# Kernel tuning notes

Hardware: AMD Instinct MI355X
Metric: run time of the kernel (lower is better)

The kernel has to match this reference:

```python
import jax, jax.numpy as jnp
import numpy as np

N_NODES = 100000
N_FEAT = 256
N_EDGES = 3200000
N_CLUSTERS = 16
COLLAPSE_REG = 0.1


def setup_inputs() -> dict:
    key = jax.random.key(0)
    k1, k2, k3, k4 = jax.random.split(key, 4)
    features = jax.random.normal(k1, (N_NODES, N_FEAT), dtype=jnp.float32)
    edge_row = jax.random.randint(k2, (N_EDGES,), 0, N_NODES, dtype=jnp.int32)
    edge_col = jax.random.randint(k3, (N_EDGES,), 0, N_NODES, dtype=jnp.int32)
    edge_val = jnp.ones((N_EDGES,), dtype=jnp.float32)
    # orthogonal-ish init approximated by scaled normal (init does not affect math)
    W = jax.random.normal(k4, (N_FEAT, N_CLUSTERS), dtype=jnp.float32) / np.float32(np.sqrt(N_FEAT))
    b = jnp.zeros((N_CLUSTERS,), dtype=jnp.float32)
    return {"features": features, "W": W, "b": b,
            "edge_row": edge_row, "edge_col": edge_col, "edge_val": edge_val}


def reference(features, W, b, edge_row, edge_col, edge_val):
    n = features.shape[0]
    k = W.shape[1]
    # assignment softmax (dropout_rate=0 -> identity)
    assignments = jax.nn.softmax(features @ W + b, axis=1)  # [n, k]
    cluster_sizes = assignments.sum(axis=0)                  # [k]
    assignments_pooling = assignments / cluster_sizes        # [n, k]
    # degrees = sparse row sums of adjacency
    degrees = jax.ops.segment_sum(edge_val, edge_row, num_segments=n)[:, None]  # [n, 1]
    n_edges = degrees.sum() / 2
    # sparse mm: adjacency @ assignments via gather + segment_sum
    adj_assign = jax.ops.segment_sum(edge_val[:, None] * assignments[edge_col],
                                     edge_row, num_segments=n)  # [n, k]
    graph_pooled = assignments.T @ adj_assign                # [k, k]
    normalizer_left = assignments.T @ degrees                # [k, 1]
    normalizer_right = degrees.T @ assignments               # [1, k]
    normalizer = normalizer_left @ normalizer_right / (2 * n_edges)
    spectral_loss = -jnp.trace(graph_pooled - normalizer) / (2 * n_edges)
    collapse_loss = COLLAPSE_REG * (jnp.linalg.norm(cluster_sizes) / n
                                    * jnp.sqrt(jnp.float32(k)) - 1.0)
    features_pooled = jax.nn.selu(assignments_pooling.T @ features)  # [k, d]
    return features_pooled, assignments, spectral_loss, collapse_loss
```

## Files before the change

kernel.cpp:

```cpp
#include <hip/hip_runtime.h>
#include <math.h>

#define KC 16
#define DF 256

#define WS_POOLED 0
#define WS_CS     4096
#define WS_M      4112
#define WS_TR     4128
#define WS_ESUM   4129
#define WS_TOTAL  4130
#define SHDW_OFF_BYTES 16640


typedef float floatx2 __attribute__((ext_vector_type(2)));

__global__ void zero_ws_kernel(float* __restrict__ ws) {
  int i = blockIdx.x * blockDim.x + threadIdx.x;
  if (i < WS_TOTAL) ws[i] = 0.0f;
}

__device__ __forceinline__ void cvt16_fp8(uint4 u, float* f) {
  floatx2 p;
  p = __builtin_amdgcn_cvt_pk_f32_fp8(u.x, false); f[0] = p[0];  f[1] = p[1];
  p = __builtin_amdgcn_cvt_pk_f32_fp8(u.x, true);  f[2] = p[0];  f[3] = p[1];
  p = __builtin_amdgcn_cvt_pk_f32_fp8(u.y, false); f[4] = p[0];  f[5] = p[1];
  p = __builtin_amdgcn_cvt_pk_f32_fp8(u.y, true);  f[6] = p[0];  f[7] = p[1];
  p = __builtin_amdgcn_cvt_pk_f32_fp8(u.z, false); f[8] = p[0];  f[9] = p[1];
  p = __builtin_amdgcn_cvt_pk_f32_fp8(u.z, true);  f[10] = p[0]; f[11] = p[1];
  p = __builtin_amdgcn_cvt_pk_f32_fp8(u.w, false); f[12] = p[0]; f[13] = p[1];
  p = __builtin_amdgcn_cvt_pk_f32_fp8(u.w, true);  f[14] = p[0]; f[15] = p[1];
}

__device__ __forceinline__ void acc_edge1(uint4 A, uint4 B, float vq,
                                          float* m, float& tr, float& es) {
  float a[16], bb[16];
  cvt16_fp8(A, a); cvt16_fp8(B, bb);
  float d = 0.f;
  #pragma unroll
  for (int k = 0; k < 16; ++k) d += a[k] * bb[k];
  tr += vq * d; es += vq;
  #pragma unroll
  for (int k = 0; k < 16; ++k) m[k] += vq * a[k];
}

__global__ void __launch_bounds__(256, 2) assign_kernel(
    const float* __restrict__ F, const float* __restrict__ W,
    const float* __restrict__ b, float* __restrict__ S,
    unsigned* __restrict__ Sh, float* __restrict__ ws, int n) {
  __shared__ float Ft[2][32 * 257];
  __shared__ float cs_l[KC];
  const int t = threadIdx.x;
  if (t < KC) cs_l[t] = 0.0f;
  const int nb = blockIdx.x << 8;
  const int node = nb + t;
  const bool valid = node < n;
  const bool interior = (nb + 256 <= n);

  const int nl = t >> 3;
  const int jc = t & 7;

  float4 pref[8];
  auto load_chunk = [&](int s) {
    #pragma unroll
    for (int it = 0; it < 8; ++it) {
      const int nn = nl + (it << 5);
      if (interior || nb + nn < n)
        pref[it] = *(const float4*)&F[(size_t)(nb + nn) * DF + (s << 5) + (jc << 2)];
      else
        pref[it] = make_float4(0.f, 0.f, 0.f, 0.f);
    }
  };

  float acc[KC];
  #pragma unroll
  for (int k = 0; k < KC; ++k) acc[k] = 0.f;

  load_chunk(0);
  for (int s = 0; s < 8; ++s) {
    float* __restrict__ B = Ft[s & 1];
    #pragma unroll
    for (int it = 0; it < 8; ++it) {
      const int nn = nl + (it << 5);
      const int d0 = jc << 2;
      B[(d0 + 0) * 257 + nn] = pref[it].x;
      B[(d0 + 1) * 257 + nn] = pref[it].y;
      B[(d0 + 2) * 257 + nn] = pref[it].z;
      B[(d0 + 3) * 257 + nn] = pref[it].w;
    }
    __syncthreads();
    if (s < 7) load_chunk(s + 1);
    #pragma unroll
    for (int j = 0; j < 8; ++j) {
      const float fv0 = B[(4 * j + 0) * 257 + t];
      const float fv1 = B[(4 * j + 1) * 257 + t];
      const float fv2 = B[(4 * j + 2) * 257 + t];
      const float fv3 = B[(4 * j + 3) * 257 + t];
      const float* __restrict__ Wg = &W[(size_t)((s << 5) + (j << 2)) * KC];
      #pragma unroll
      for (int k = 0; k < KC; ++k)
        acc[k] += fv0 * Wg[k] + fv1 * Wg[KC + k]
                + fv2 * Wg[2 * KC + k] + fv3 * Wg[3 * KC + k];
    }
  }

  float mx = -1e30f;
  #pragma unroll
  for (int k = 0; k < KC; ++k) { acc[k] += b[k]; mx = fmaxf(mx, acc[k]); }
  float sum = 0.f;
  #pragma unroll
  for (int k = 0; k < KC; ++k) { acc[k] = __expf(acc[k] - mx); sum += acc[k]; }
  const float inv = 1.0f / sum;
  #pragma unroll
  for (int k = 0; k < KC; ++k) acc[k] *= inv;
  if (!valid) {
    #pragma unroll
    for (int k = 0; k < KC; ++k) acc[k] = 0.f;
  }
  if (valid) {
    float4* __restrict__ So = (float4*)&S[(size_t)node * KC];
    So[0] = make_float4(acc[0],  acc[1],  acc[2],  acc[3]);
    So[1] = make_float4(acc[4],  acc[5],  acc[6],  acc[7]);
    So[2] = make_float4(acc[8],  acc[9],  acc[10], acc[11]);
    So[3] = make_float4(acc[12], acc[13], acc[14], acc[15]);
    if (Sh) {
      unsigned w0, w1, w2, w3;
      w0 = __builtin_amdgcn_cvt_pk_fp8_f32(acc[0],  acc[1],  0,  false);
      w0 = __builtin_amdgcn_cvt_pk_fp8_f32(acc[2],  acc[3],  w0, true);
      w1 = __builtin_amdgcn_cvt_pk_fp8_f32(acc[4],  acc[5],  0,  false);
      w1 = __builtin_amdgcn_cvt_pk_fp8_f32(acc[6],  acc[7],  w1, true);
      w2 = __builtin_amdgcn_cvt_pk_fp8_f32(acc[8],  acc[9],  0,  false);
      w2 = __builtin_amdgcn_cvt_pk_fp8_f32(acc[10], acc[11], w2, true);
      w3 = __builtin_amdgcn_cvt_pk_fp8_f32(acc[12], acc[13], 0,  false);
      w3 = __builtin_amdgcn_cvt_pk_fp8_f32(acc[14], acc[15], w3, true);
      *(uint4*)&Sh[(size_t)node * 4] = make_uint4(w0, w1, w2, w3);
    }
  }
  #pragma unroll
  for (int off = 1; off < 64; off <<= 1) {
    #pragma unroll
    for (int k = 0; k < KC; ++k) acc[k] += __shfl_xor(acc[k], off);
  }
  if ((t & 63) == 0) {
    #pragma unroll
    for (int k = 0; k < KC; ++k) atomicAdd(&cs_l[k], acc[k]);
  }
  __syncthreads();
  if (t < KC) atomicAdd(&ws[WS_CS + t], cs_l[t]);
}

__device__ __forceinline__ void edge_body_fp8(
    const int* __restrict__ erow, const int* __restrict__ ecol,
    const float* __restrict__ evl, const uint4* __restrict__ S8,
    float* __restrict__ ws, int ne, int idx, float* __restrict__ red) {
  const int t = threadIdx.x;
  if (t < KC + 2) red[t] = 0.0f;
  __syncthreads();

  float m[KC];
  #pragma unroll
  for (int i = 0; i < KC; ++i) m[i] = 0.f;
  float tr = 0.f, es = 0.f;

  const int cbase = idx << 11;
  const int base = cbase + t;
  int r[8], c[8];
  float v[8];
  if (cbase + 2048 <= ne) {
    #pragma unroll
    for (int i = 0; i < 8; ++i) {
      const int e = base + (i << 8);
      r[i] = erow[e]; c[i] = ecol[e]; v[i] = evl[e];
    }
  } else {
    #pragma unroll
    for (int i = 0; i < 8; ++i) {
      const int e = base + (i << 8);
      const bool ok = e < ne;
      r[i] = ok ? erow[e] : 0;
      c[i] = ok ? ecol[e] : 0;
      v[i] = ok ? evl[e] : 0.f;
    }
  }

  const uint4 A0 = S8[r[0]], B0 = S8[c[0]], A1 = S8[r[1]], B1 = S8[c[1]],
              A2 = S8[r[2]], B2 = S8[c[2]], A3 = S8[r[3]], B3 = S8[c[3]],
              A4 = S8[r[4]], B4 = S8[c[4]], A5 = S8[r[5]], B5 = S8[c[5]],
              A6 = S8[r[6]], B6 = S8[c[6]], A7 = S8[r[7]], B7 = S8[c[7]];
  acc_edge1(A0, B0, v[0], m, tr, es);
  acc_edge1(A1, B1, v[1], m, tr, es);
  acc_edge1(A2, B2, v[2], m, tr, es);
  acc_edge1(A3, B3, v[3], m, tr, es);
  acc_edge1(A4, B4, v[4], m, tr, es);
  acc_edge1(A5, B5, v[5], m, tr, es);
  acc_edge1(A6, B6, v[6], m, tr, es);
  acc_edge1(A7, B7, v[7], m, tr, es);

  #pragma unroll
  for (int off = 1; off < 64; off <<= 1) {
    tr += __shfl_xor(tr, off);
    es += __shfl_xor(es, off);
    #pragma unroll
    for (int i = 0; i < KC; ++i) m[i] += __shfl_xor(m[i], off);
  }
  if ((t & 63) == 0) {
    atomicAdd(&red[KC], tr);
    atomicAdd(&red[KC + 1], es);
    #pragma unroll
    for (int i = 0; i < KC; ++i) atomicAdd(&red[i], m[i]);
  }
  __syncthreads();
  if (t < KC)            atomicAdd(&ws[WS_M + t], red[t]);
  else if (t == KC)      atomicAdd(&ws[WS_TR], red[KC]);
  else if (t == KC + 1)  atomicAdd(&ws[WS_ESUM], red[KC + 1]);
}

__device__ __forceinline__ void pool_body(
    const float* __restrict__ F, const float* __restrict__ S,
    float* __restrict__ ws, int n, int idx, int pg) {
  const int t = threadIdx.x;
  float acc[KC];
  #pragma unroll
  for (int i = 0; i < KC; ++i) acc[i] = 0.f;

  const int nch = n >> 5;
  for (int ch = idx; ch < nch; ch += pg) {
    const int base = ch << 5;
    float fl[32];
    #pragma unroll
    for (int i = 0; i < 32; ++i)
      fl[i] = F[(size_t)(base + i) * DF + t];
    #pragma unroll
    for (int i = 0; i < 32; ++i) {
      const float4* __restrict__ Sr = (const float4*)(S + (size_t)(base + i) * KC);
      const float4 s0 = Sr[0], s1 = Sr[1], s2 = Sr[2], s3 = Sr[3];
      const float f = fl[i];
      acc[0]+=f*s0.x;  acc[1]+=f*s0.y;  acc[2]+=f*s0.z;  acc[3]+=f*s0.w;
      acc[4]+=f*s1.x;  acc[5]+=f*s1.y;  acc[6]+=f*s1.z;  acc[7]+=f*s1.w;
      acc[8]+=f*s2.x;  acc[9]+=f*s2.y;  acc[10]+=f*s2.z; acc[11]+=f*s2.w;
      acc[12]+=f*s3.x; acc[13]+=f*s3.y; acc[14]+=f*s3.z; acc[15]+=f*s3.w;
    }
  }
  if (idx == 0) {
    for (int i2 = nch << 5; i2 < n; ++i2) {
      const float f = F[(size_t)i2 * DF + t];
      const float* __restrict__ Sr = S + (size_t)i2 * KC;
      #pragma unroll
      for (int kk = 0; kk < KC; ++kk) acc[kk] += f * Sr[kk];
    }
  }
  const int rot = idx & 15;
  #pragma unroll
  for (int kk = 0; kk < KC; ++kk) {
    const int kidx = (kk + rot) & 15;
    atomicAdd(&ws[WS_POOLED + kidx * DF + t], acc[kidx]);
  }
}

__global__ void __launch_bounds__(256) edge_pool_kernel(
    const int* __restrict__ erow, const int* __restrict__ ecol,
    const float* __restrict__ evl, const uint4* __restrict__ S8,
    const float* __restrict__ F, const float* __restrict__ S,
    float* __restrict__ ws, int ne, int n, int pg, int eg) {
  __shared__ float red[KC + 2];
  const int bid = blockIdx.x;
  const int mn = pg < eg ? pg : eg;
  const int nInter = 2 * mn;
  int role, idx;
  if (bid < nInter) { role = bid & 1; idx = bid >> 1; }
  else {
    const int rem = bid - nInter;
    role = (pg > eg) ? 0 : 1;
    idx = mn + rem;
  }
  if (role == 0) pool_body(F, S, ws, n, idx, pg);
  else           edge_body_fp8(erow, ecol, evl, S8, ws, ne, idx, red);
}

__global__ void __launch_bounds__(256) edge_kernel_f32(
    const int* __restrict__ erow, const int* __restrict__ ecol,
    const float* __restrict__ evl, const float* __restrict__ S,
    float* __restrict__ ws, int ne) {
  __shared__ float red[KC + 2];
  const int t = threadIdx.x;
  if (t < KC + 2) red[t] = 0.0f;
  __syncthreads();
  float m[KC];
  #pragma unroll
  for (int i = 0; i < KC; ++i) m[i] = 0.f;
  float tr = 0.f, es = 0.f;
  const int stride = gridDim.x * blockDim.x;
  for (int e = blockIdx.x * blockDim.x + t; e < ne; e += stride) {
    const int r = erow[e];
    const int c = ecol[e];
    const float v = evl[e];
    const float4* __restrict__ Sr = (const float4*)(S + (size_t)r * KC);
    const float4* __restrict__ Sc = (const float4*)(S + (size_t)c * KC);
    const float4 a0 = Sr[0], a1 = Sr[1], a2 = Sr[2], a3 = Sr[3];
    const float4 b0 = Sc[0], b1 = Sc[1], b2 = Sc[2], b3 = Sc[3];
    float d = a0.x*b0.x + a0.y*b0.y + a0.z*b0.z + a0.w*b0.w
            + a1.x*b1.x + a1.y*b1.y + a1.z*b1.z + a1.w*b1.w
            + a2.x*b2.x + a2.y*b2.y + a2.z*b2.z + a2.w*b2.w
            + a3.x*b3.x + a3.y*b3.y + a3.z*b3.z + a3.w*b3.w;
    tr += v * d; es += v;
    m[0]+=v*a0.x; m[1]+=v*a0.y; m[2]+=v*a0.z; m[3]+=v*a0.w;
    m[4]+=v*a1.x; m[5]+=v*a1.y; m[6]+=v*a1.z; m[7]+=v*a1.w;
    m[8]+=v*a2.x; m[9]+=v*a2.y; m[10]+=v*a2.z; m[11]+=v*a2.w;
    m[12]+=v*a3.x; m[13]+=v*a3.y; m[14]+=v*a3.z; m[15]+=v*a3.w;
  }
  #pragma unroll
  for (int off = 1; off < 64; off <<= 1) {
    tr += __shfl_xor(tr, off);
    es += __shfl_xor(es, off);
    #pragma unroll
    for (int i = 0; i < KC; ++i) m[i] += __shfl_xor(m[i], off);
  }
  if ((t & 63) == 0) {
    atomicAdd(&red[KC], tr);
    atomicAdd(&red[KC + 1], es);
    #pragma unroll
    for (int i = 0; i < KC; ++i) atomicAdd(&red[i], m[i]);
  }
  __syncthreads();
  if (t < KC)            atomicAdd(&ws[WS_M + t], red[t]);
  else if (t == KC)      atomicAdd(&ws[WS_TR], red[KC]);
  else if (t == KC + 1)  atomicAdd(&ws[WS_ESUM], red[KC + 1]);
}

__global__ void finalize_kernel(const float* __restrict__ ws,
                                float* __restrict__ out, int n) {
  const int idx = blockIdx.x * 256 + threadIdx.x;
  const float alpha = 1.6732632423543772f;
  const float scale = 1.0507009873554805f;
  if (idx < KC * DF) {
    const int k = idx >> 8;
    const float x = ws[WS_POOLED + idx] / ws[WS_CS + k];
    const float r = x > 0.f ? x : alpha * expm1f(x);
    out[idx] = scale * r;
  }
  if (idx == 0) {
    const float esum = ws[WS_ESUM];
    const float tr = ws[WS_TR];
    float sm2 = 0.f, sc2 = 0.f;
    for (int i = 0; i < KC; ++i) {
      const float mi = ws[WS_M + i];
      sm2 += mi * mi;
      const float ci = ws[WS_CS + i];
      sc2 += ci * ci;
    }
    const float spectral = -(tr - sm2 / esum) / esum;
    const float collapse = 0.1f * (sqrtf(sc2) / (float)n * 4.0f - 1.0f);
    const size_t off = (size_t)(KC * DF) + (size_t)n * KC;
    out[off] = spectral;
    out[off + 1] = collapse;
  }
}

extern "C" void kernel_launch(void* const* d_in, const int* in_sizes, int n_in,
                              void* d_out, int out_size, void* d_ws, size_t ws_size,
                              hipStream_t stream) {
  const float* F   = (const float*)d_in[0];
  const float* W   = (const float*)d_in[1];
  const float* b   = (const float*)d_in[2];
  const int* erow  = (const int*)d_in[3];
  const int* ecol  = (const int*)d_in[4];
  const float* evl = (const float*)d_in[5];
  const int n  = in_sizes[0] / DF;
  const int ne = in_sizes[3];
  float* out = (float*)d_out;
  float* S   = out + KC * DF;
  float* ws  = (float*)d_ws;

  const size_t shadow_bytes = (size_t)n * 16;
  const bool use_shadow = ws_size >= (size_t)SHDW_OFF_BYTES + shadow_bytes + 64;
  unsigned* Sh = use_shadow ? (unsigned*)((char*)d_ws + SHDW_OFF_BYTES) : nullptr;

  zero_ws_kernel<<<(WS_TOTAL + 255) / 256, 256, 0, stream>>>(ws);
  assign_kernel<<<(n + 255) / 256, 256, 0, stream>>>(F, W, b, S, Sh, ws, n);

  const int pg = 2048;
  if (use_shadow) {
    const int eg = (ne + 2047) >> 11;
    edge_pool_kernel<<<pg + eg, 256, 0, stream>>>(
        erow, ecol, evl, (const uint4*)Sh, F, S, ws, ne, n, pg, eg);
  } else {
    edge_kernel_f32<<<2048, 256, 0, stream>>>(erow, ecol, evl, S, ws, ne);
    edge_pool_kernel<<<pg, 256, 0, stream>>>(
        erow, ecol, evl, (const uint4*)nullptr, F, S, ws, ne, n, pg, 0);
  }
  finalize_kernel<<<16, 256, 0, stream>>>(ws, out, n);
}
```

Before: 290.4 us.

## Replace LDS-transposed feature tiling with four-threads-per-node direct row reads

The assignment GEMV kernel no longer stages feature chunks through a double-buffered shared-memory transpose. Instead, four lanes share each node: each lane reads a contiguous 64-float slice of the row as float4 loads, and the four partial results are combined with two xor shuffles. Each lane then writes one float4 of the softmax output and one fp8 word of the shadow copy, and the grid is launched with four times as many blocks. This removes the LDS traffic, the block barriers and the occupancy limit from shared memory, at the cost of strided per-instruction global loads and softmax work repeated in all four lanes.

```diff
diff --git a/kernel.cpp b/kernel.cpp
--- a/kernel.cpp
+++ b/kernel.cpp
@@ -44,64 +44,41 @@
   for (int k = 0; k < 16; ++k) m[k] += vq * a[k];
 }
 
-__global__ void __launch_bounds__(256, 2) assign_kernel(
+__global__ void __launch_bounds__(256) assign_kernel(
     const float* __restrict__ F, const float* __restrict__ W,
     const float* __restrict__ b, float* __restrict__ S,
     unsigned* __restrict__ Sh, float* __restrict__ ws, int n) {
-  __shared__ float Ft[2][32 * 257];
   __shared__ float cs_l[KC];
   const int t = threadIdx.x;
   if (t < KC) cs_l[t] = 0.0f;
-  const int nb = blockIdx.x << 8;
-  const int node = nb + t;
+  __syncthreads();
+
+  const int nl = t >> 2;
+  const int q  = t & 3;
+  const int node = (blockIdx.x << 6) + nl;
   const bool valid = node < n;
-  const bool interior = (nb + 256 <= n);
-
-  const int nl = t >> 3;
-  const int jc = t & 7;
-
-  float4 pref[8];
-  auto load_chunk = [&](int s) {
-    #pragma unroll
-    for (int it = 0; it < 8; ++it) {
-      const int nn = nl + (it << 5);
-      if (interior || nb + nn < n)
-        pref[it] = *(const float4*)&F[(size_t)(nb + nn) * DF + (s << 5) + (jc << 2)];
-      else
-        pref[it] = make_float4(0.f, 0.f, 0.f, 0.f);
-    }
-  };
 
   float acc[KC];
   #pragma unroll
   for (int k = 0; k < KC; ++k) acc[k] = 0.f;
 
-  load_chunk(0);
-  for (int s = 0; s < 8; ++s) {
-    float* __restrict__ B = Ft[s & 1];
-    #pragma unroll
-    for (int it = 0; it < 8; ++it) {
-      const int nn = nl + (it << 5);
-      const int d0 = jc << 2;
-      B[(d0 + 0) * 257 + nn] = pref[it].x;
-      B[(d0 + 1) * 257 + nn] = pref[it].y;
-      B[(d0 + 2) * 257 + nn] = pref[it].z;
-      B[(d0 + 3) * 257 + nn] = pref[it].w;
-    }
-    __syncthreads();
-    if (s < 7) load_chunk(s + 1);
-    #pragma unroll
-    for (int j = 0; j < 8; ++j) {
-      const float fv0 = B[(4 * j + 0) * 257 + t];
-      const float fv1 = B[(4 * j + 1) * 257 + t];
-      const float fv2 = B[(4 * j + 2) * 257 + t];
-      const float fv3 = B[(4 * j + 3) * 257 + t];
-      const float* __restrict__ Wg = &W[(size_t)((s << 5) + (j << 2)) * KC];
+  if (valid) {
+    const float4* __restrict__ Fr =
+        (const float4*)&F[(size_t)node * DF + (q << 6)];
+    #pragma unroll
+    for (int i = 0; i < 16; ++i) {
+      const float4 fv = Fr[i];
+      const float* __restrict__ Wg = &W[(size_t)((q << 6) + (i << 2)) * KC];
       #pragma unroll
       for (int k = 0; k < KC; ++k)
-        acc[k] += fv0 * Wg[k] + fv1 * Wg[KC + k]
-                + fv2 * Wg[2 * KC + k] + fv3 * Wg[3 * KC + k];
-    }
+        acc[k] += fv.x * Wg[k] + fv.y * Wg[KC + k]
+                + fv.z * Wg[2 * KC + k] + fv.w * Wg[3 * KC + k];
+    }
+  }
+  #pragma unroll
+  for (int k = 0; k < KC; ++k) {
+    acc[k] += __shfl_xor(acc[k], 1);
+    acc[k] += __shfl_xor(acc[k], 2);
   }
 
   float mx = -1e30f;
@@ -117,27 +94,26 @@
     #pragma unroll
     for (int k = 0; k < KC; ++k) acc[k] = 0.f;
   }
+
   if (valid) {
-    float4* __restrict__ So = (float4*)&S[(size_t)node * KC];
-    So[0] = make_float4(acc[0],  acc[1],  acc[2],  acc[3]);
-    So[1] = make_float4(acc[4],  acc[5],  acc[6],  acc[7]);
-    So[2] = make_float4(acc[8],  acc[9],  acc[10], acc[11]);
-    So[3] = make_float4(acc[12], acc[13], acc[14], acc[15]);
+    float o0, o1, o2, o3;
+    switch (q) {
+      case 0:  o0 = acc[0];  o1 = acc[1];  o2 = acc[2];  o3 = acc[3];  break;
+      case 1:  o0 = acc[4];  o1 = acc[5];  o2 = acc[6];  o3 = acc[7];  break;
+      case 2:  o0 = acc[8];  o1 = acc[9];  o2 = acc[10]; o3 = acc[11]; break;
+      default: o0 = acc[12]; o1 = acc[13]; o2 = acc[14]; o3 = acc[15]; break;
+    }
+    ((float4*)&S[(size_t)node * KC])[q] = make_float4(o0, o1, o2, o3);
     if (Sh) {
-      unsigned w0, w1, w2, w3;
-      w0 = __builtin_amdgcn_cvt_pk_fp8_f32(acc[0],  acc[1],  0,  false);
-      w0 = __builtin_amdgcn_cvt_pk_fp8_f32(acc[2],  acc[3],  w0, true);
-      w1 = __builtin_amdgcn_cvt_pk_fp8_f32(acc[4],  acc[5],  0,  false);
-      w1 = __builtin_amdgcn_cvt_pk_fp8_f32(acc[6],  acc[7],  w1, true);
-      w2 = __builtin_amdgcn_cvt_pk_fp8_f32(acc[8],  acc[9],  0,  false);
-      w2 = __builtin_amdgcn_cvt_pk_fp8_f32(acc[10], acc[11], w2, true);
-      w3 = __builtin_amdgcn_cvt_pk_fp8_f32(acc[12], acc[13], 0,  false);
-      w3 = __builtin_amdgcn_cvt_pk_fp8_f32(acc[14], acc[15], w3, true);
-      *(uint4*)&Sh[(size_t)node * 4] = make_uint4(w0, w1, w2, w3);
-    }
-  }
-  #pragma unroll
-  for (int off = 1; off < 64; off <<= 1) {
+      unsigned wp;
+      wp = __builtin_amdgcn_cvt_pk_fp8_f32(o0, o1, 0,  false);
+      wp = __builtin_amdgcn_cvt_pk_fp8_f32(o2, o3, wp, true);
+      Sh[(size_t)node * 4 + q] = wp;
+    }
+  }
+
+  #pragma unroll
+  for (int off = 4; off < 64; off <<= 1) {
     #pragma unroll
     for (int k = 0; k < KC; ++k) acc[k] += __shfl_xor(acc[k], off);
   }
@@ -376,7 +352,8 @@
   unsigned* Sh = use_shadow ? (unsigned*)((char*)d_ws + SHDW_OFF_BYTES) : nullptr;
 
   zero_ws_kernel<<<(WS_TOTAL + 255) / 256, 256, 0, stream>>>(ws);
-  assign_kernel<<<(n + 255) / 256, 256, 0, stream>>>(F, W, b, S, Sh, ws, n);
+  const int ag = (n + 63) >> 6;
+  assign_kernel<<<ag, 256, 0, stream>>>(F, W, b, S, Sh, ws, n);
 
   const int pg = 2048;
   if (use_shadow) {
```

Measured after the change: 465.8 us. 60.4% more time.

## Fuse all phases into one cooperative persistent kernel with grid syncs

Applied to the files above, without the earlier changes.

Merges the assign, edge/pool and finalize stages into one cooperative kernel, using grid-wide syncs in place of separate launches. The zero-init kernel becomes a hipMemsetAsync. After the first sync, each block splits its threads: half do feature pooling, half run a grid-strided edge loop. This removes launch gaps and tail effects between kernels. In exchange, each phase gets only about 391 blocks of 256 threads, fewer than the 2048+ blocks before, and grid syncs add cost. If the cooperative launch fails, the old multi-kernel path is used.

```diff
diff --git a/kernel.cpp b/kernel.cpp
--- a/kernel.cpp
+++ b/kernel.cpp
@@ -1,5 +1,8 @@
 #include <hip/hip_runtime.h>
+#include <hip/hip_cooperative_groups.h>
 #include <math.h>
+
+namespace cg = cooperative_groups;
 
 #define KC 16
 #define DF 256
@@ -14,11 +17,6 @@
 
 
 typedef float floatx2 __attribute__((ext_vector_type(2)));
-
-__global__ void zero_ws_kernel(float* __restrict__ ws) {
-  int i = blockIdx.x * blockDim.x + threadIdx.x;
-  if (i < WS_TOTAL) ws[i] = 0.0f;
-}
 
 __device__ __forceinline__ void cvt16_fp8(uint4 u, float* f) {
   floatx2 p;
@@ -44,12 +42,12 @@
   for (int k = 0; k < 16; ++k) m[k] += vq * a[k];
 }
 
-__global__ void __launch_bounds__(256, 2) assign_kernel(
+__device__ __forceinline__ void assign_phase(
     const float* __restrict__ F, const float* __restrict__ W,
     const float* __restrict__ b, float* __restrict__ S,
-    unsigned* __restrict__ Sh, float* __restrict__ ws, int n) {
-  __shared__ float Ft[2][32 * 257];
-  __shared__ float cs_l[KC];
+    unsigned* __restrict__ Sh, float* __restrict__ ws, int n,
+    float* __restrict__ Ft0, float* __restrict__ Ft1,
+    float* __restrict__ cs_l) {
   const int t = threadIdx.x;
   if (t < KC) cs_l[t] = 0.0f;
   const int nb = blockIdx.x << 8;
@@ -78,7 +76,7 @@
 
   load_chunk(0);
   for (int s = 0; s < 8; ++s) {
-    float* __restrict__ B = Ft[s & 1];
+    float* __restrict__ B = (s & 1) ? Ft1 : Ft0;
     #pragma unroll
     for (int it = 0; it < 8; ++it) {
       const int nn = nl + (it << 5);
@@ -149,6 +147,195 @@
   if (t < KC) atomicAdd(&ws[WS_CS + t], cs_l[t]);
 }
 
+__device__ __forceinline__ void pool_role128(
+    const float* __restrict__ F, const float* __restrict__ S,
+    float* __restrict__ ws, int n, int bid, int nb) {
+  const int t = threadIdx.x;
+  float acc0[KC], acc1[KC];
+  #pragma unroll
+  for (int i = 0; i < KC; ++i) { acc0[i] = 0.f; acc1[i] = 0.f; }
+
+  const int nch = n >> 5;
+  for (int ch = bid; ch < nch; ch += nb) {
+    const int base = ch << 5;
+    float fl[32];
+    #pragma unroll
+    for (int i = 0; i < 32; ++i)
+      fl[i] = F[(size_t)(base + i) * DF + t];
+    #pragma unroll
+    for (int i = 0; i < 32; ++i) {
+      const float4* __restrict__ Sr = (const float4*)(S + (size_t)(base + i) * KC);
+      const float4 s0 = Sr[0], s1 = Sr[1], s2 = Sr[2], s3 = Sr[3];
+      const float f = fl[i];
+      acc0[0]+=f*s0.x;  acc0[1]+=f*s0.y;  acc0[2]+=f*s0.z;  acc0[3]+=f*s0.w;
+      acc0[4]+=f*s1.x;  acc0[5]+=f*s1.y;  acc0[6]+=f*s1.z;  acc0[7]+=f*s1.w;
+      acc0[8]+=f*s2.x;  acc0[9]+=f*s2.y;  acc0[10]+=f*s2.z; acc0[11]+=f*s2.w;
+      acc0[12]+=f*s3.x; acc0[13]+=f*s3.y; acc0[14]+=f*s3.z; acc0[15]+=f*s3.w;
+    }
+    #pragma unroll
+    for (int i = 0; i < 32; ++i)
+      fl[i] = F[(size_t)(base + i) * DF + t + 128];
+    #pragma unroll
+    for (int i = 0; i < 32; ++i) {
+      const float4* __restrict__ Sr = (const float4*)(S + (size_t)(base + i) * KC);
+      const float4 s0 = Sr[0], s1 = Sr[1], s2 = Sr[2], s3 = Sr[3];
+      const float f = fl[i];
+      acc1[0]+=f*s0.x;  acc1[1]+=f*s0.y;  acc1[2]+=f*s0.z;  acc1[3]+=f*s0.w;
+      acc1[4]+=f*s1.x;  acc1[5]+=f*s1.y;  acc1[6]+=f*s1.z;  acc1[7]+=f*s1.w;
+      acc1[8]+=f*s2.x;  acc1[9]+=f*s2.y;  acc1[10]+=f*s2.z; acc1[11]+=f*s2.w;
+      acc1[12]+=f*s3.x; acc1[13]+=f*s3.y; acc1[14]+=f*s3.z; acc1[15]+=f*s3.w;
+    }
+  }
+  if (bid == 0) {
+    for (int i2 = nch << 5; i2 < n; ++i2) {
+      const float f0 = F[(size_t)i2 * DF + t];
+      const float f1 = F[(size_t)i2 * DF + t + 128];
+      const float* __restrict__ Sr = S + (size_t)i2 * KC;
+      #pragma unroll
+      for (int kk = 0; kk < KC; ++kk) {
+        acc0[kk] += f0 * Sr[kk];
+        acc1[kk] += f1 * Sr[kk];
+      }
+    }
+  }
+  const int rot = bid & 15;
+  #pragma unroll
+  for (int kk = 0; kk < KC; ++kk) {
+    const int kidx = (kk + rot) & 15;
+    atomicAdd(&ws[WS_POOLED + kidx * DF + t], acc0[kidx]);
+    atomicAdd(&ws[WS_POOLED + kidx * DF + t + 128], acc1[kidx]);
+  }
+}
+
+__device__ __forceinline__ void edge_role128(
+    const int* __restrict__ erow, const int* __restrict__ ecol,
+    const float* __restrict__ evl, const uint4* __restrict__ S8,
+    float* __restrict__ ws, int ne, int bid, int nb) {
+  const int t = threadIdx.x;
+  const int l = t - 128;
+  float m[KC];
+  #pragma unroll
+  for (int i = 0; i < KC; ++i) m[i] = 0.f;
+  float tr = 0.f, es = 0.f;
+
+  for (long long cb = (long long)bid << 13; cb < ne;
+       cb += (long long)nb << 13) {
+    #pragma unroll
+    for (int i = 0; i < 8; ++i) {
+      const long long b0 = cb + (i << 10);
+      if (b0 >= ne) break;
+      int r[8], c[8];
+      float v[8];
+      if (b0 + 1024 <= ne) {
+        #pragma unroll
+        for (int j = 0; j < 8; ++j) {
+          const int e = (int)b0 + l + (j << 7);
+          r[j] = erow[e]; c[j] = ecol[e]; v[j] = evl[e];
+        }
+      } else {
+        #pragma unroll
+        for (int j = 0; j < 8; ++j) {
+          const long long e = b0 + l + (j << 7);
+          const bool ok = e < ne;
+          r[j] = ok ? erow[e] : 0;
+          c[j] = ok ? ecol[e] : 0;
+          v[j] = ok ? evl[e] : 0.f;
+        }
+      }
+      const uint4 A0 = S8[r[0]], B0 = S8[c[0]], A1 = S8[r[1]], B1 = S8[c[1]],
+                  A2 = S8[r[2]], B2 = S8[c[2]], A3 = S8[r[3]], B3 = S8[c[3]],
+                  A4 = S8[r[4]], B4 = S8[c[4]], A5 = S8[r[5]], B5 = S8[c[5]],
+                  A6 = S8[r[6]], B6 = S8[c[6]], A7 = S8[r[7]], B7 = S8[c[7]];
+      acc_edge1(A0, B0, v[0], m, tr, es);
+      acc_edge1(A1, B1, v[1], m, tr, es);
+      acc_edge1(A2, B2, v[2], m, tr, es);
+      acc_edge1(A3, B3, v[3], m, tr, es);
+      acc_edge1(A4, B4, v[4], m, tr, es);
+      acc_edge1(A5, B5, v[5], m, tr, es);
+      acc_edge1(A6, B6, v[6], m, tr, es);
+      acc_edge1(A7, B7, v[7], m, tr, es);
+    }
+  }
+  #pragma unroll
+  for (int off = 1; off < 64; off <<= 1) {
+    tr += __shfl_xor(tr, off);
+    es += __shfl_xor(es, off);
+    #pragma unroll
+    for (int i = 0; i < KC; ++i) m[i] += __shfl_xor(m[i], off);
+  }
+  if ((t & 63) == 0) {
+    atomicAdd(&ws[WS_TR], tr);
+    atomicAdd(&ws[WS_ESUM], es);
+    #pragma unroll
+    for (int i = 0; i < KC; ++i) atomicAdd(&ws[WS_M + i], m[i]);
+  }
+}
+
+__device__ __forceinline__ void finalize_plain(const float* __restrict__ ws,
+                                               float* __restrict__ out, int n,
+                                               float* __restrict__ s_cs) {
+  const int t = threadIdx.x;
+  if (t < KC) s_cs[t] = ws[WS_CS + t];
+  __syncthreads();
+  const float alpha = 1.6732632423543772f;
+  const float scale = 1.0507009873554805f;
+  for (int idx = t; idx < KC * DF; idx += 256) {
+    const int k = idx >> 8;
+    const float x = ws[WS_POOLED + idx] / s_cs[k];
+    const float r = x > 0.f ? x : alpha * expm1f(x);
+    out[idx] = scale * r;
+  }
+  if (t == 0) {
+    const float esum = ws[WS_ESUM];
+    const float tr = ws[WS_TR];
+    float sm2 = 0.f, sc2 = 0.f;
+    for (int i = 0; i < KC; ++i) {
+      const float mi = ws[WS_M + i];
+      sm2 += mi * mi;
+      const float ci = s_cs[i];
+      sc2 += ci * ci;
+    }
+    const float spectral = -(tr - sm2 / esum) / esum;
+    const float collapse = 0.1f * (sqrtf(sc2) / (float)n * 4.0f - 1.0f);
+    const size_t off = (size_t)(KC * DF) + (size_t)n * KC;
+    out[off] = spectral;
+    out[off + 1] = collapse;
+  }
+}
+
+__global__ void __launch_bounds__(256, 2) fused_all_kernel(
+    const float* __restrict__ F, const float* __restrict__ W,
+    const float* __restrict__ b, float* __restrict__ S,
+    unsigned* __restrict__ Sh, const int* __restrict__ erow,
+    const int* __restrict__ ecol, const float* __restrict__ evl,
+    float* __restrict__ ws, float* __restrict__ out, int n, int ne) {
+  __shared__ float Ft[2][32 * 257];
+  __shared__ float cs_l[KC];
+
+  assign_phase(F, W, b, S, Sh, ws, n, Ft[0], Ft[1], cs_l);
+
+  cg::this_grid().sync();
+
+  const int nb = gridDim.x;
+  if (threadIdx.x < 128)
+    pool_role128(F, S, ws, n, blockIdx.x, nb);
+  else
+    edge_role128(erow, ecol, evl, (const uint4*)Sh, ws, ne, blockIdx.x, nb);
+
+  cg::this_grid().sync();
+
+  if (blockIdx.x == 0) finalize_plain(ws, out, n, cs_l);
+}
+
+__global__ void __launch_bounds__(256, 2) assign_kernel(
+    const float* __restrict__ F, const float* __restrict__ W,
+    const float* __restrict__ b, float* __restrict__ S,
+    unsigned* __restrict__ Sh, float* __restrict__ ws, int n) {
+  __shared__ float Ft[2][32 * 257];
+  __shared__ float cs_l[KC];
+  assign_phase(F, W, b, S, Sh, ws, n, Ft[0], Ft[1], cs_l);
+}
+
 __device__ __forceinline__ void edge_body_fp8(
     const int* __restrict__ erow, const int* __restrict__ ecol,
     const float* __restrict__ evl, const uint4* __restrict__ S8,
@@ -156,12 +343,10 @@
   const int t = threadIdx.x;
   if (t < KC + 2) red[t] = 0.0f;
   __syncthreads();
-
   float m[KC];
   #pragma unroll
   for (int i = 0; i < KC; ++i) m[i] = 0.f;
   float tr = 0.f, es = 0.f;
-
   const int cbase = idx << 11;
   const int base = cbase + t;
   int r[8], c[8];
@@ -182,7 +367,6 @@
       v[i] = ok ? evl[e] : 0.f;
     }
   }
-
   const uint4 A0 = S8[r[0]], B0 = S8[c[0]], A1 = S8[r[1]], B1 = S8[c[1]],
               A2 = S8[r[2]], B2 = S8[c[2]], A3 = S8[r[3]], B3 = S8[c[3]],
               A4 = S8[r[4]], B4 = S8[c[4]], A5 = S8[r[5]], B5 = S8[c[5]],
@@ -195,7 +379,6 @@
   acc_edge1(A5, B5, v[5], m, tr, es);
   acc_edge1(A6, B6, v[6], m, tr, es);
   acc_edge1(A7, B7, v[7], m, tr, es);
-
   #pragma unroll
   for (int off = 1; off < 64; off <<= 1) {
     tr += __shfl_xor(tr, off);
@@ -222,7 +405,6 @@
   float acc[KC];
   #pragma unroll
   for (int i = 0; i < KC; ++i) acc[i] = 0.f;
-
   const int nch = n >> 5;
   for (int ch = idx; ch < nch; ch += pg) {
     const int base = ch << 5;
@@ -329,31 +511,8 @@
 
 __global__ void finalize_kernel(const float* __restrict__ ws,
                                 float* __restrict__ out, int n) {
-  const int idx = blockIdx.x * 256 + threadIdx.x;
-  const float alpha = 1.6732632423543772f;
-  const float scale = 1.0507009873554805f;
-  if (idx < KC * DF) {
-    const int k = idx >> 8;
-    const float x = ws[WS_POOLED + idx] / ws[WS_CS + k];
-    const float r = x > 0.f ? x : alpha * expm1f(x);
-    out[idx] = scale * r;
-  }
-  if (idx == 0) {
-    const float esum = ws[WS_ESUM];
-    const float tr = ws[WS_TR];
-    float sm2 = 0.f, sc2 = 0.f;
-    for (int i = 0; i < KC; ++i) {
-      const float mi = ws[WS_M + i];
-      sm2 += mi * mi;
-      const float ci = ws[WS_CS + i];
-      sc2 += ci * ci;
-    }
-    const float spectral = -(tr - sm2 / esum) / esum;
-    const float collapse = 0.1f * (sqrtf(sc2) / (float)n * 4.0f - 1.0f);
-    const size_t off = (size_t)(KC * DF) + (size_t)n * KC;
-    out[off] = spectral;
-    out[off + 1] = collapse;
-  }
+  __shared__ float s_cs[KC];
+  finalize_plain(ws, out, n, s_cs);
 }
 
 extern "C" void kernel_launch(void* const* d_in, const int* in_sizes, int n_in,
@@ -365,8 +524,8 @@
   const int* erow  = (const int*)d_in[3];
   const int* ecol  = (const int*)d_in[4];
   const float* evl = (const float*)d_in[5];
-  const int n  = in_sizes[0] / DF;
-  const int ne = in_sizes[3];
+  int n  = in_sizes[0] / DF;
+  int ne = in_sizes[3];
   float* out = (float*)d_out;
   float* S   = out + KC * DF;
   float* ws  = (float*)d_ws;
@@ -375,18 +534,30 @@
   const bool use_shadow = ws_size >= (size_t)SHDW_OFF_BYTES + shadow_bytes + 64;
   unsigned* Sh = use_shadow ? (unsigned*)((char*)d_ws + SHDW_OFF_BYTES) : nullptr;
 
-  zero_ws_kernel<<<(WS_TOTAL + 255) / 256, 256, 0, stream>>>(ws);
-  assign_kernel<<<(n + 255) / 256, 256, 0, stream>>>(F, W, b, S, Sh, ws, n);
-
-  const int pg = 2048;
-  if (use_shadow) {
-    const int eg = (ne + 2047) >> 11;
-    edge_pool_kernel<<<pg + eg, 256, 0, stream>>>(
-        erow, ecol, evl, (const uint4*)Sh, F, S, ws, ne, n, pg, eg);
-  } else {
-    edge_kernel_f32<<<2048, 256, 0, stream>>>(erow, ecol, evl, S, ws, ne);
-    edge_pool_kernel<<<pg, 256, 0, stream>>>(
-        erow, ecol, evl, (const uint4*)nullptr, F, S, ws, ne, n, pg, 0);
-  }
-  finalize_kernel<<<16, 256, 0, stream>>>(ws, out, n);
-}
+  hipMemsetAsync(d_ws, 0, WS_TOTAL * sizeof(float), stream);
+
+  const int ag = (n + 255) >> 8;
+  bool done = false;
+  if (use_shadow && ag <= 512) {
+    void* args[] = {(void*)&F, (void*)&W, (void*)&b, (void*)&S, (void*)&Sh,
+                    (void*)&erow, (void*)&ecol, (void*)&evl,
+                    (void*)&ws, (void*)&out, (void*)&n, (void*)&ne};
+    hipError_t err = hipLaunchCooperativeKernel(
+        (const void*)fused_all_kernel, dim3(ag), dim3(256), args, 0, stream);
+    done = (err == hipSuccess);
+  }
+  if (!done) {
+    assign_kernel<<<ag, 256, 0, stream>>>(F, W, b, S, Sh, ws, n);
+    const int pg = 2048;
+    if (use_shadow) {
+      const int eg = (ne + 2047) >> 11;
+      edge_pool_kernel<<<pg + eg, 256, 0, stream>>>(
+          erow, ecol, evl, (const uint4*)Sh, F, S, ws, ne, n, pg, eg);
+    } else {
+      edge_kernel_f32<<<2048, 256, 0, stream>>>(erow, ecol, evl, S, ws, ne);
+      edge_pool_kernel<<<pg, 256, 0, stream>>>(
+          erow, ecol, evl, (const uint4*)nullptr, F, S, ws, ne, n, pg, 0);
+    }
+    finalize_kernel<<<1, 256, 0, stream>>>(ws, out, n);
+  }
+}
```

Result: slower. 502.0 us (+72.9%).
